# Kernel tuning notes

Measured on AMD Instinct MI355X. Metric: run time of the kernel, lower is better.

The kernel has to match this reference:

```python
import jax, jax.numpy as jnp
import numpy as np

N_WIRES = 4
N_LAYERS = 2
B = 16384
EPS = 1e-5


def apply_ry(state, wire, theta):
    # state: (B,2,2,2,2) complex64; theta: scalar or (B,)
    st = jnp.moveaxis(state, wire + 1, 1)
    half = jnp.asarray(theta) * 0.5
    c = jnp.cos(half).reshape(-1, 1, 1, 1).astype(state.dtype)
    s = jnp.sin(half).reshape(-1, 1, 1, 1).astype(state.dtype)
    n0 = c * st[:, 0] - s * st[:, 1]
    n1 = s * st[:, 0] + c * st[:, 1]
    return jnp.moveaxis(jnp.stack([n0, n1], axis=1), 1, wire + 1)


def apply_rz(state, wire, theta):
    st = jnp.moveaxis(state, wire + 1, 1)
    half = jnp.asarray(theta) * 0.5
    c = jnp.cos(half)
    s = jnp.sin(half)
    p0 = (c - 1j * s).reshape(-1, 1, 1, 1).astype(state.dtype)
    p1 = (c + 1j * s).reshape(-1, 1, 1, 1).astype(state.dtype)
    return jnp.moveaxis(jnp.stack([p0 * st[:, 0], p1 * st[:, 1]], axis=1), 1, wire + 1)


def apply_cnot(state, ctrl, tgt):
    st = jnp.moveaxis(state, (ctrl + 1, tgt + 1), (1, 2))
    # flip target where control == 1
    st = jnp.concatenate([st[:, :1], st[:, 1:, ::-1]], axis=1)
    return jnp.moveaxis(st, (1, 2), (ctrl + 1, tgt + 1))


def expect_z(state):
    probs = jnp.real(state * jnp.conj(state))  # (B,2,2,2,2)
    exps = []
    for w in range(N_WIRES):
        p = jnp.moveaxis(probs, w + 1, 1)
        exps.append((p[:, 0] - p[:, 1]).sum(axis=(1, 2, 3)))
    return jnp.stack(exps, axis=-1)  # (B,4)


def quanv(x, qparams):
    bsz = x.shape[0]
    # 2x2 patches in row-major loop order: (B, 196, 4) with [p00,p01,p10,p11]
    patches = x.reshape(bsz, 14, 2, 14, 2).transpose(0, 1, 3, 2, 4).reshape(bsz, 196, 4)
    patches = jnp.transpose(patches, (1, 0, 2))  # (196, B, 4)
    state0 = jnp.zeros((bsz, 2, 2, 2, 2), jnp.complex64).at[:, 0, 0, 0, 0].set(1.0)

    def step(state, vals):
        # NOTE: original code never resets the device between patches -> state carries over
        for i in range(N_WIRES):
            state = apply_ry(state, i, vals[:, i])
        for l in range(N_LAYERS):
            for i in range(N_WIRES):
                state = apply_ry(state, i, qparams[l, i, 0])
                state = apply_rz(state, i, qparams[l, i, 1])
            for i in range(N_WIRES - 1):
                state = apply_cnot(state, i, i + 1)
        return state, expect_z(state)

    _, meas = jax.lax.scan(step, state0, patches)  # (196, B, 4)
    return jnp.transpose(meas, (1, 0, 2)).reshape(bsz, 196 * 4)


def batchnorm(h, g, b):
    # training-mode BatchNorm1d: biased batch statistics
    m = h.mean(axis=0)
    v = h.var(axis=0)
    return g * (h - m) / jnp.sqrt(v + EPS) + b


def setup_inputs() -> dict:
    key = jax.random.key(0)
    ks = jax.random.split(key, 6)
    x = jax.random.uniform(ks[0], (B, 28, 28), dtype=jnp.float32)
    qparams = jax.random.normal(ks[1], (N_LAYERS, N_WIRES, 2), dtype=jnp.float32)
    w1 = jax.random.normal(ks[2], (256, 784), dtype=jnp.float32) * 0.03
    w2 = jax.random.normal(ks[3], (256, 256), dtype=jnp.float32) * 0.05
    w3 = jax.random.normal(ks[4], (10, 256), dtype=jnp.float32) * 0.05
    return {
        "x": x, "qparams": qparams,
        "w1": w1, "b1": jnp.zeros((256,), jnp.float32),
        "g1": jnp.ones((256,), jnp.float32), "be1": jnp.zeros((256,), jnp.float32),
        "w2": w2, "b2": jnp.zeros((256,), jnp.float32),
        "g2": jnp.ones((256,), jnp.float32), "be2": jnp.zeros((256,), jnp.float32),
        "w3": w3, "b3": jnp.zeros((10,), jnp.float32),
    }


def reference(x, qparams, w1, b1, g1, be1, w2, b2, g2, be2, w3, b3):
    feats = quanv(x, qparams)                      # (B, 784)
    h = jax.nn.relu(batchnorm(feats @ w1.T + b1, g1, be1))
    h2 = jax.nn.relu(batchnorm(h @ w2.T + b2, g2, be2)) + h
    return jax.nn.log_softmax(h2 @ w3.T + b3, axis=-1)
```

## Files before the change

kernel.cpp:

```cpp
#include <hip/hip_runtime.h>
#include <math.h>

#define BQ 16384
#define KFP 800
#define NH 256
#define NCLS 10

typedef float f32x4 __attribute__((ext_vector_type(4)));
typedef unsigned int u32x2 __attribute__((ext_vector_type(2)));
typedef __bf16 bf16x8 __attribute__((ext_vector_type(8)));
typedef __bf16 bf16x4 __attribute__((ext_vector_type(4)));


template<int ST>
__device__ __forceinline__ void u_ry(float* sr, float* si, float c, float s) {
#pragma unroll
  for (int i = 0; i < 16; i++) {
    if (i & ST) continue;
    const int j = i | ST;
    const float a0r = sr[i], a0i = si[i], a1r = sr[j], a1i = si[j];
    sr[i] = c * a0r - s * a1r;  si[i] = c * a0i - s * a1i;
    sr[j] = s * a0r + c * a1r;  si[j] = s * a0i + c * a1i;
  }
}
template<int ST>
__device__ __forceinline__ void u_rz(float* sr, float* si, float c, float s) {
#pragma unroll
  for (int i = 0; i < 16; i++) {
    const float pz = (i & ST) ? s : -s;
    const float ar = sr[i], ai = si[i];
    sr[i] = c * ar - pz * ai;
    si[i] = c * ai + pz * ar;
  }
}
template<int SC, int STG>
__device__ __forceinline__ void u_cnot(float* sr, float* si) {
#pragma unroll
  for (int i = 0; i < 16; i++) {
    if (!(i & SC) || (i & STG)) continue;
    const int j = i | STG;
    float t;
    t = sr[i]; sr[i] = sr[j]; sr[j] = t;
    t = si[i]; si[i] = si[j]; si[j] = t;
  }
}

__global__ __launch_bounds__(256) void prep_kernel(
    const float* __restrict__ qp, const float* __restrict__ w1,
    const float* __restrict__ w2, __bf16* __restrict__ Abuf,
    __bf16* __restrict__ w1b, __bf16* __restrict__ w2b,
    float* __restrict__ gs1, float* __restrict__ gs2) {
  const int bid = blockIdx.x;
  const int tid = threadIdx.x;
  if (bid == 0) {
    gs1[tid] = 0.f; gs1[256 + tid] = 0.f;
    gs2[tid] = 0.f; gs2[256 + tid] = 0.f;
    __shared__ float Ur[16][16], Ui[16][16];
    if (tid < 16) {
      float sr[16], si[16];
#pragma unroll
      for (int i = 0; i < 16; i++) { sr[i] = (i == tid) ? 1.f : 0.f; si[i] = 0.f; }
#pragma unroll
      for (int l = 0; l < 2; l++) {
        { const float t = qp[l*8 + 0] * 0.5f; u_ry<8>(sr, si, cosf(t), sinf(t)); }
        { const float t = qp[l*8 + 1] * 0.5f; u_rz<8>(sr, si, cosf(t), sinf(t)); }
        { const float t = qp[l*8 + 2] * 0.5f; u_ry<4>(sr, si, cosf(t), sinf(t)); }
        { const float t = qp[l*8 + 3] * 0.5f; u_rz<4>(sr, si, cosf(t), sinf(t)); }
        { const float t = qp[l*8 + 4] * 0.5f; u_ry<2>(sr, si, cosf(t), sinf(t)); }
        { const float t = qp[l*8 + 5] * 0.5f; u_rz<2>(sr, si, cosf(t), sinf(t)); }
        { const float t = qp[l*8 + 6] * 0.5f; u_ry<1>(sr, si, cosf(t), sinf(t)); }
        { const float t = qp[l*8 + 7] * 0.5f; u_rz<1>(sr, si, cosf(t), sinf(t)); }
        u_cnot<8, 4>(sr, si);
        u_cnot<4, 2>(sr, si);
        u_cnot<2, 1>(sr, si);
      }
#pragma unroll
      for (int r = 0; r < 16; r++) { Ur[r][tid] = sr[r]; Ui[r][tid] = si[r]; }
    }
    __syncthreads();
    for (int f = tid; f < 2048; f += 256) {
      const int m   = f & 7;
      const int row = (f >> 3) & 15;
      const int kg  = (f >> 7) & 3;
      const int hl  = (f >> 9) & 1;
      const int t   = (f >> 10) & 1;
      const int k   = kg * 8 + m;
      const int ri_o  = (row >> 2) & 1;
      const int amp_o = ((row >> 3) & 1) * 8 + t * 4 + (row & 3);
      const int ri_i  = (k >> 3) & 1;
      const int amp_i = ((k >> 4) & 1) * 8 + (m >> 2) * 4 + (m & 3);
      const float u_r = Ur[amp_o][amp_i], u_i = Ui[amp_o][amp_i];
      float v = (ri_o == 0) ? ((ri_i == 0) ? u_r : -u_i)
                            : ((ri_i == 0) ? u_i : u_r);
      if (hl) {
        const __bf16 hb = (__bf16)v;
        v = v - (float)hb;
      }
      Abuf[f] = (__bf16)v;
    }
  } else if (bid <= 256) {
    const int r = bid - 1;
    for (int c = tid; c < KFP; c += 256)
      w1b[r * KFP + c] = (c < 784) ? (__bf16)w1[r * 784 + c] : (__bf16)0.f;
  } else {
    const int base = (bid - 257) * 2048 + tid * 8;
    const float4 v0 = *(const float4*)(w2 + base);
    const float4 v1 = *(const float4*)(w2 + base + 4);
    bf16x8 o = {(__bf16)v0.x, (__bf16)v0.y, (__bf16)v0.z, (__bf16)v0.w,
                (__bf16)v1.x, (__bf16)v1.y, (__bf16)v1.z, (__bf16)v1.w};
    *(bf16x8*)(w2b + base) = o;
  }
}


__device__ __forceinline__ float swz16(float v) {
  return __int_as_float(__builtin_amdgcn_ds_swizzle(__float_as_int(v), 0x401F));
}
__device__ __forceinline__ float plsum(float v) {
  const u32x2 r = __builtin_amdgcn_permlane32_swap(
      __float_as_uint(v), __float_as_uint(v), false, false);
  return __uint_as_float(r.x) + __uint_as_float(r.y);
}
__device__ __forceinline__ float plpick(float v, bool r0sel) {
  const u32x2 r = __builtin_amdgcn_permlane32_swap(
      __float_as_uint(v), __float_as_uint(v), false, false);
  return __uint_as_float(r0sel ? r.x : r.y);
}

__global__ __launch_bounds__(256) void quanv_mfma(
    const float* __restrict__ x, const __bf16* __restrict__ Abuf,
    __bf16* __restrict__ feats) {
  const int tid = threadIdx.x;
  const int l = tid & 63;
  const int wv = tid >> 6;
  const int col = l & 15;
  const int kg = l >> 4;
  const int b = blockIdx.x * 64 + wv * 16 + col;
  const float* xb = x + (size_t)b * 784;
  __bf16* fb = feats + (size_t)b * KFP;
  const float sg0 = (l & 32) ? 1.f : -1.f;

  const u32x2 pt = __builtin_amdgcn_permlane32_swap((unsigned)l, (unsigned)l,
                                                    false, false);
  const bool p32r0 = (pt.x == (unsigned)(l ^ 32));

  const bf16x8* Ab = (const bf16x8*)Abuf;
  const bf16x8 A0h = Ab[(0 * 4 + kg) * 16 + col];
  const bf16x8 A0l = Ab[(1 * 4 + kg) * 16 + col];
  const bf16x8 A1h = Ab[(2 * 4 + kg) * 16 + col];
  const bf16x8 A1l = Ab[(3 * 4 + kg) * 16 + col];

  f32x4 c0 = {(kg == 0) ? 1.f : 0.f, 0.f, 0.f, 0.f};
  f32x4 c1 = {0.f, 0.f, 0.f, 0.f};
  const f32x4 z4 = {0.f, 0.f, 0.f, 0.f};

  float ts0, tw1, tw2, tw3, gsc;
  auto trig = [&](float2 a, float2 b2) {
    const float h0 = a.x * 0.5f, h1 = a.y * 0.5f;
    const float h2 = b2.x * 0.5f, h3 = b2.y * 0.5f;
    const float c0_ = __cosf(h0), s0_ = __sinf(h0);
    const float c1_ = __cosf(h1), s1_ = __sinf(h1);
    const float c2_ = __cosf(h2), s2_ = __sinf(h2);
    const float c3_ = __cosf(h3), s3_ = __sinf(h3);
    ts0 = sg0 * __fdividef(s0_, c0_);
    tw1 = __fdividef(s1_, c1_);
    tw2 = __fdividef(s2_, c2_);
    tw3 = __fdividef(s3_, c3_);
    gsc = (c0_ * c1_) * (c2_ * c3_);
  };

  auto meas = [&](__bf16* dst) {
    const float sq0 = c0.x * c0.x, sq1 = c0.y * c0.y;
    const float sq2 = c0.z * c0.z, sq3 = c0.w * c0.w;
    const float sq4 = c1.x * c1.x, sq5 = c1.y * c1.y;
    const float sq6 = c1.z * c1.z, sq7 = c1.w * c1.w;
    const float s01 = sq0 + sq1, s23 = sq2 + sq3;
    const float s45 = sq4 + sq5, s67 = sq6 + sq7;
    const float d01 = sq0 - sq1, d23 = sq2 - sq3;
    const float d45 = sq4 - sq5, d67 = sq6 - sq7;
    const float z3 = (d01 + d23) + (d45 + d67);
    const float z2 = (s01 - s23) + (s45 - s67);
    const float q03 = s01 + s23, q47 = s45 + s67;
    const float z1 = q03 - q47;
    const float T  = q03 + q47;
    const float z3a = z3 + swz16(z3);
    const float z2a = z2 + swz16(z2);
    const float z1a = z1 + swz16(z1);
    const float Ta  = -sg0 * (T + swz16(T));
    const float z3f = plsum(z3a);
    const float z2f = plsum(z2a);
    const float z1f = plsum(z1a);
    const float z0f = plsum(Ta);
    if (kg == 0) {
      bf16x4 o = {(__bf16)z0f, (__bf16)z1f, (__bf16)z2f, (__bf16)z3f};
      *(bf16x4*)dst = o;
    }
  };

  auto step = [&]() {
    float S[8] = {c0.x, c0.y, c0.z, c0.w, c1.x, c1.y, c1.z, c1.w};
#pragma unroll
    for (int j = 0; j < 4; j++) {
      const float a = S[j];
      S[j]     = fmaf(-tw1, S[4 + j], S[j]);
      S[4 + j] = fmaf( tw1, a,        S[4 + j]);
    }
#pragma unroll
    for (int base = 0; base < 8; base += 4)
#pragma unroll
      for (int j = 0; j < 2; j++) {
        const int i0 = base + j, i1 = base + j + 2;
        const float a = S[i0];
        S[i0] = fmaf(-tw2, S[i1], S[i0]);
        S[i1] = fmaf( tw2, a,     S[i1]);
      }
#pragma unroll
    for (int i0 = 0; i0 < 8; i0 += 2) {
      const float a = S[i0];
      S[i0]     = fmaf(-tw3, S[i0 + 1], S[i0]);
      S[i0 + 1] = fmaf( tw3, a,         S[i0 + 1]);
    }
#pragma unroll
    for (int i = 0; i < 8; i++) {
      const float P = plpick(S[i], p32r0);
      S[i] = fmaf(ts0, P, S[i]);
    }
    bf16x8 Bh, Bl;
#pragma unroll
    for (int i = 0; i < 8; i++) {
      const float GS = gsc * S[i];
      const __bf16 hb = (__bf16)GS;
      Bh[i] = hb;
      Bl[i] = (__bf16)(GS - (float)hb);
    }
    f32x4 p0 = __builtin_amdgcn_mfma_f32_16x16x32_bf16(A0h, Bh, z4, 0, 0, 0);
    f32x4 q0 = __builtin_amdgcn_mfma_f32_16x16x32_bf16(A0l, Bh, z4, 0, 0, 0);
    q0 = __builtin_amdgcn_mfma_f32_16x16x32_bf16(A0h, Bl, q0, 0, 0, 0);
    f32x4 p1 = __builtin_amdgcn_mfma_f32_16x16x32_bf16(A1h, Bh, z4, 0, 0, 0);
    f32x4 q1 = __builtin_amdgcn_mfma_f32_16x16x32_bf16(A1l, Bh, z4, 0, 0, 0);
    q1 = __builtin_amdgcn_mfma_f32_16x16x32_bf16(A1h, Bl, q1, 0, 0, 0);
    c0 = p0 + q0;
    c1 = p1 + q1;
  };

  float2 t0 = *(const float2*)(xb);
  float2 t1 = *(const float2*)(xb + 28);
  trig(t0, t1);
  t0 = *(const float2*)(xb + 2);
  t1 = *(const float2*)(xb + 30);
  step();
  trig(t0, t1);
  t0 = *(const float2*)(xb + 4);
  t1 = *(const float2*)(xb + 32);
  int nrr = 0, ncc = 3;
  __bf16* fp = fb;

#pragma unroll 2
  for (int it = 1; it < 196; ++it) {
    const float* np = (it < 194) ? (xb + 56 * nrr + 2 * ncc) : xb;
    const float2 n0 = *(const float2*)np;
    const float2 n1 = *(const float2*)(np + 28);
    ncc++;
    if (ncc == 14) { ncc = 0; nrr++; }

    meas(fp); fp += 4;
    step();
    trig(t0, t1);
    t0 = n0; t1 = n1;
  }
  meas(fp);

  if (kg == 0) {
    *(uint4*)(fb + 784) = (uint4){0, 0, 0, 0};
    *(uint4*)(fb + 792) = (uint4){0, 0, 0, 0};
  }
}

#define GBM 128
#define GBN 64
#define GBK 32

__device__ __forceinline__ void gld16(const void* g, void* l) {
  __builtin_amdgcn_global_load_lds(
      (const __attribute__((address_space(1))) unsigned int*)g,
      (__attribute__((address_space(3))) unsigned int*)l, 16, 0, 0);
}

__global__ __launch_bounds__(256) void gemm_bf16_nt(
    const __bf16* __restrict__ A, const __bf16* __restrict__ B,
    const float* __restrict__ bias, float* __restrict__ C,
    int M, int N, int K, float* __restrict__ gstats) {
  __shared__ char lds[24576];
  const int tid = threadIdx.x;
  const int nwg = gridDim.x;
  const int sid = (blockIdx.x & 7) * (nwg >> 3) + (blockIdx.x >> 3);
  const int bm = (sid >> 2) * GBM;
  const int bn = (sid & 3) * GBN;
  const int NK = K / GBK;
  const size_t lda = (size_t)K * 2;

  const int srow = tid >> 2;
  const int lc16 = tid & 3;
  const int ag0 = lc16 ^ ((srow >> 1) & 3);
  const int ag1 = lc16 ^ (((srow + 64) >> 1) & 3);
  const char* a0p = (const char*)A + (size_t)(bm + srow) * lda + ag0 * 16;
  const char* a1p = (const char*)A + (size_t)(bm + 64 + srow) * lda + ag1 * 16;
  const char* b0p = (const char*)B + (size_t)(bn + srow) * lda + ag0 * 16;

  const int wid = tid >> 6, lane = tid & 63;
  const int wr = wid >> 1, wc = wid & 1;
  const int ln15 = lane & 15, ln4 = lane >> 4;
  int aoff[4], boff[2];
#pragma unroll
  for (int m = 0; m < 4; m++) {
    const int row = wr * 64 + m * 16 + ln15;
    aoff[m] = row * 64 + ((ln4 ^ ((row >> 1) & 3)) * 16);
  }
#pragma unroll
  for (int n = 0; n < 2; n++) {
    const int row = wc * 32 + n * 16 + ln15;
    boff[n] = 16384 + row * 64 + ((ln4 ^ ((row >> 1) & 3)) * 16);
  }

  f32x4 acc[4][2];
#pragma unroll
  for (int m = 0; m < 4; m++)
#pragma unroll
    for (int n = 0; n < 2; n++) acc[m][n] = (f32x4){0.f, 0.f, 0.f, 0.f};

  auto stage = [&](int buf, int kt) {
    const size_t kb = (size_t)kt * GBK * 2;
    char* as = lds + buf * 8192 + tid * 16;
    char* bs = lds + 16384 + buf * 4096 + tid * 16;
    gld16(a0p + kb, as);
    gld16(a1p + kb, as + 4096);
    gld16(b0p + kb, bs);
  };

  stage(0, 0);
  for (int kt = 0; kt < NK; kt++) {
    __syncthreads();
    if (kt + 1 < NK) stage((kt + 1) & 1, kt + 1);
    const int ab = (kt & 1) * 8192, bb = (kt & 1) * 4096;
    bf16x8 af[4], bfr[2];
#pragma unroll
    for (int m = 0; m < 4; m++) af[m] = *(const bf16x8*)(lds + ab + aoff[m]);
#pragma unroll
    for (int n = 0; n < 2; n++) bfr[n] = *(const bf16x8*)(lds + bb + boff[n]);
#pragma unroll
    for (int m = 0; m < 4; m++)
#pragma unroll
      for (int n = 0; n < 2; n++)
        acc[m][n] = __builtin_amdgcn_mfma_f32_16x16x32_bf16(af[m], bfr[n], acc[m][n], 0, 0, 0);
  }

  float csum[2], csq[2];
#pragma unroll
  for (int n = 0; n < 2; n++) {
    const int ccol = bn + wc * 32 + n * 16 + ln15;
    const float bv = bias[ccol];
    float s = 0.f, ss = 0.f;
#pragma unroll
    for (int m = 0; m < 4; m++) {
      const int crow = bm + wr * 64 + m * 16 + ln4 * 4;
#pragma unroll
      for (int r = 0; r < 4; r++) {
        const float v = acc[m][n][r] + bv;
        C[(size_t)(crow + r) * N + ccol] = v;
        s += v; ss += v * v;
      }
    }
    csum[n] = s; csq[n] = ss;
  }
  __syncthreads();
  float* sred = (float*)lds;
#pragma unroll
  for (int n = 0; n < 2; n++) {
    const int slot = wid * 128 + ln4 * 32 + n * 16 + ln15;
    sred[slot] = csum[n];
    sred[512 + slot] = csq[n];
  }
  __syncthreads();
  if (tid < 128) {
    const int colb = tid & 63, which = tid >> 6;
    const int wcc = colb >> 5, c31 = colb & 31;
    float a = 0.f;
    const int base = which * 512 + c31;
#pragma unroll
    for (int w2_ = 0; w2_ < 2; w2_++)
#pragma unroll
      for (int l4 = 0; l4 < 4; l4++)
        a += sred[base + (w2_ * 2 + wcc) * 128 + l4 * 32];
    atomicAdd(&gstats[(bn + colb) * 2 + which], a);
  }
}

__global__ __launch_bounds__(256) void bn_finalize_g(
    const float* __restrict__ gstats, const float* __restrict__ g,
    const float* __restrict__ be, float* __restrict__ ab, float* __restrict__ cb) {
  const int t = threadIdx.x;
  const float s = gstats[t * 2], ss = gstats[t * 2 + 1];
  const float mean = s * (1.f / 16384.f);
  const float var = ss * (1.f / 16384.f) - mean * mean;
  const float rstd = rsqrtf(var + 1e-5f);
  const float a = g[t] * rstd;
  ab[t] = a;
  cb[t] = be[t] - mean * a;
}

__global__ __launch_bounds__(256) void bn_relu_cvt(
    const float* __restrict__ h, __bf16* __restrict__ hb,
    const float* __restrict__ ab, const float* __restrict__ cb) {
  const size_t i = (size_t)blockIdx.x * 256 + threadIdx.x;
  const float4 v = ((const float4*)h)[i];
  const int col = (int)((i * 4) & (NH - 1));
  const float4 a = *(const float4*)(ab + col);
  const float4 c = *(const float4*)(cb + col);
  bf16x4 o = {(__bf16)fmaxf(fmaf(v.x, a.x, c.x), 0.f),
              (__bf16)fmaxf(fmaf(v.y, a.y, c.y), 0.f),
              (__bf16)fmaxf(fmaf(v.z, a.z, c.z), 0.f),
              (__bf16)fmaxf(fmaf(v.w, a.w, c.w), 0.f)};
  *(bf16x4*)(hb + i * 4) = o;
}

__global__ __launch_bounds__(256) void tail_fused(
    const float* __restrict__ h2p, const __bf16* __restrict__ h1b,
    const float* __restrict__ ab, const float* __restrict__ cb,
    const float* __restrict__ w3, const float* __restrict__ b3,
    float* __restrict__ out) {
  __shared__ float w3s[NCLS * NH];
  __shared__ float as[NH], cs[NH];
  for (int i = threadIdx.x; i < NCLS * NH; i += 256) w3s[i] = w3[i];
  as[threadIdx.x] = ab[threadIdx.x];
  cs[threadIdx.x] = cb[threadIdx.x];
  __syncthreads();

  const int m = blockIdx.x * 256 + threadIdx.x;
  const float* hr = h2p + (size_t)m * NH;
  const __bf16* rr = h1b + (size_t)m * NH;
  float acc[NCLS];
#pragma unroll
  for (int n = 0; n < NCLS; n++) acc[n] = b3[n];

  for (int k = 0; k < NH; k += 8) {
    const float4 hv0 = *(const float4*)(hr + k);
    const float4 hv1 = *(const float4*)(hr + k + 4);
    const bf16x8 rv = *(const bf16x8*)(rr + k);
    float v[8] = {hv0.x, hv0.y, hv0.z, hv0.w, hv1.x, hv1.y, hv1.z, hv1.w};
#pragma unroll
    for (int j = 0; j < 8; j++)
      v[j] = fmaxf(fmaf(v[j], as[k + j], cs[k + j]), 0.f) + (float)rv[j];
#pragma unroll
    for (int n = 0; n < NCLS; n++) {
      float d = 0.f;
#pragma unroll
      for (int j = 0; j < 8; j++) d = fmaf(v[j], w3s[n * NH + k + j], d);
      acc[n] += d;
    }
  }

  float mx = acc[0];
#pragma unroll
  for (int n = 1; n < NCLS; n++) mx = fmaxf(mx, acc[n]);
  float se = 0.f;
#pragma unroll
  for (int n = 0; n < NCLS; n++) se += expf(acc[n] - mx);
  const float lse = logf(se) + mx;
#pragma unroll
  for (int n = 0; n < NCLS; n++) out[(size_t)m * NCLS + n] = acc[n] - lse;
}

extern "C" void kernel_launch(void* const* d_in, const int* in_sizes, int n_in,
                              void* d_out, int out_size, void* d_ws, size_t ws_size,
                              hipStream_t stream) {
  const float* x   = (const float*)d_in[0];
  const float* qp  = (const float*)d_in[1];
  const float* w1  = (const float*)d_in[2];
  const float* b1  = (const float*)d_in[3];
  const float* g1  = (const float*)d_in[4];
  const float* be1 = (const float*)d_in[5];
  const float* w2  = (const float*)d_in[6];
  const float* b2  = (const float*)d_in[7];
  const float* g2  = (const float*)d_in[8];
  const float* be2 = (const float*)d_in[9];
  const float* w3  = (const float*)d_in[10];
  const float* b3  = (const float*)d_in[11];
  float* out = (float*)d_out;

  char* w = (char*)d_ws;
  __bf16* feats = (__bf16*)w;
  float*  h1    = (float*)(w + 26214400);
  float*  h2p   = (float*)(w + 42991616);
  __bf16* h1b   = (__bf16*)(w + 59768832);
  __bf16* w1b   = (__bf16*)(w + 68157440);
  __bf16* w2b   = (__bf16*)(w + 68567040);
  float*  gs1   = (float*)(w + 68698112);
  float*  gs2   = (float*)(w + 68700160);
  float*  ab1   = (float*)(w + 68702208);
  float*  cb1   = (float*)(w + 68703232);
  float*  ab2   = (float*)(w + 68704256);
  float*  cb2   = (float*)(w + 68705280);
  __bf16* Abuf  = (__bf16*)(w + 68706304);

  prep_kernel<<<289, 256, 0, stream>>>(qp, w1, w2, Abuf, w1b, w2b, gs1, gs2);
  quanv_mfma<<<BQ / 64, 256, 0, stream>>>(x, Abuf, feats);

  gemm_bf16_nt<<<(BQ / GBM) * (NH / GBN), 256, 0, stream>>>(
      feats, w1b, b1, h1, BQ, NH, KFP, gs1);
  bn_finalize_g<<<1, 256, 0, stream>>>(gs1, g1, be1, ab1, cb1);
  bn_relu_cvt<<<(BQ * NH / 4) / 256, 256, 0, stream>>>(h1, h1b, ab1, cb1);

  gemm_bf16_nt<<<(BQ / GBM) * (NH / GBN), 256, 0, stream>>>(
      h1b, w2b, b2, h2p, BQ, NH, NH, gs2);
  bn_finalize_g<<<1, 256, 0, stream>>>(gs2, g2, be2, ab2, cb2);

  tail_fused<<<BQ / 256, 256, 0, stream>>>(h2p, h1b, ab2, cb2, w3, b3, out);
}
```

Measured before the change: 202.4 us.

## Interleave two independent quanv sample groups per wavefront to hide serial latency

The quanv kernel now has each 64-lane wavefront process two groups of 16 samples at once, interleaving their measure/step/trig chains. Previously each wave carried one serial dependency chain of MFMA, permlane and trig work across 196 patches. Interleaving two independent chains is meant to let one group's MFMA and cross-lane latency overlap with the other's ALU work. Launch geometry changes from 256-thread blocks of 64 samples to 64-thread blocks of 32 samples, so the total wave count halves and register pressure per wave rises, which can reduce occupancy.

```diff
diff --git a/kernel.cpp b/kernel.cpp
--- a/kernel.cpp
+++ b/kernel.cpp
@@ -127,17 +127,116 @@
   return __uint_as_float(r0sel ? r.x : r.y);
 }
 
-__global__ __launch_bounds__(256) void quanv_mfma(
+struct QGrp {
+  f32x4 c0, c1;
+  float ts0, tw1, tw2, tw3, gsc;
+  float2 t0, t1;
+  const float* xb;
+  __bf16* fb;
+};
+
+__device__ __forceinline__ void q_trig(QGrp& g, float2 a, float2 b2, float sg0) {
+  const float h0 = a.x * 0.5f, h1 = a.y * 0.5f;
+  const float h2 = b2.x * 0.5f, h3 = b2.y * 0.5f;
+  const float c0_ = __cosf(h0), s0_ = __sinf(h0);
+  const float c1_ = __cosf(h1), s1_ = __sinf(h1);
+  const float c2_ = __cosf(h2), s2_ = __sinf(h2);
+  const float c3_ = __cosf(h3), s3_ = __sinf(h3);
+  g.ts0 = sg0 * __fdividef(s0_, c0_);
+  g.tw1 = __fdividef(s1_, c1_);
+  g.tw2 = __fdividef(s2_, c2_);
+  g.tw3 = __fdividef(s3_, c3_);
+  g.gsc = (c0_ * c1_) * (c2_ * c3_);
+}
+
+__device__ __forceinline__ void q_meas(const QGrp& g, __bf16* dst,
+                                       float sg0, int kg) {
+  const f32x4 c0 = g.c0, c1 = g.c1;
+  const float sq0 = c0.x * c0.x, sq1 = c0.y * c0.y;
+  const float sq2 = c0.z * c0.z, sq3 = c0.w * c0.w;
+  const float sq4 = c1.x * c1.x, sq5 = c1.y * c1.y;
+  const float sq6 = c1.z * c1.z, sq7 = c1.w * c1.w;
+  const float s01 = sq0 + sq1, s23 = sq2 + sq3;
+  const float s45 = sq4 + sq5, s67 = sq6 + sq7;
+  const float d01 = sq0 - sq1, d23 = sq2 - sq3;
+  const float d45 = sq4 - sq5, d67 = sq6 - sq7;
+  const float z3 = (d01 + d23) + (d45 + d67);
+  const float z2 = (s01 - s23) + (s45 - s67);
+  const float q03 = s01 + s23, q47 = s45 + s67;
+  const float z1 = q03 - q47;
+  const float T  = q03 + q47;
+  const float z3a = z3 + swz16(z3);
+  const float z2a = z2 + swz16(z2);
+  const float z1a = z1 + swz16(z1);
+  const float Ta  = -sg0 * (T + swz16(T));
+  const float z3f = plsum(z3a);
+  const float z2f = plsum(z2a);
+  const float z1f = plsum(z1a);
+  const float z0f = plsum(Ta);
+  if (kg == 0) {
+    bf16x4 o = {(__bf16)z0f, (__bf16)z1f, (__bf16)z2f, (__bf16)z3f};
+    *(bf16x4*)dst = o;
+  }
+}
+
+__device__ __forceinline__ void q_step(QGrp& g, bool p32r0,
+                                       bf16x8 A0h, bf16x8 A0l,
+                                       bf16x8 A1h, bf16x8 A1l) {
+  const f32x4 z4 = {0.f, 0.f, 0.f, 0.f};
+  float S[8] = {g.c0.x, g.c0.y, g.c0.z, g.c0.w,
+                g.c1.x, g.c1.y, g.c1.z, g.c1.w};
+#pragma unroll
+  for (int j = 0; j < 4; j++) {
+    const float a = S[j];
+    S[j]     = fmaf(-g.tw1, S[4 + j], S[j]);
+    S[4 + j] = fmaf( g.tw1, a,        S[4 + j]);
+  }
+#pragma unroll
+  for (int base = 0; base < 8; base += 4)
+#pragma unroll
+    for (int j = 0; j < 2; j++) {
+      const int i0 = base + j, i1 = base + j + 2;
+      const float a = S[i0];
+      S[i0] = fmaf(-g.tw2, S[i1], S[i0]);
+      S[i1] = fmaf( g.tw2, a,     S[i1]);
+    }
+#pragma unroll
+  for (int i0 = 0; i0 < 8; i0 += 2) {
+    const float a = S[i0];
+    S[i0]     = fmaf(-g.tw3, S[i0 + 1], S[i0]);
+    S[i0 + 1] = fmaf( g.tw3, a,         S[i0 + 1]);
+  }
+#pragma unroll
+  for (int i = 0; i < 8; i++) {
+    const float P = plpick(S[i], p32r0);
+    S[i] = fmaf(g.ts0, P, S[i]);
+  }
+  bf16x8 Bh, Bl;
+#pragma unroll
+  for (int i = 0; i < 8; i++) {
+    const float GS = g.gsc * S[i];
+    const __bf16 hb = (__bf16)GS;
+    Bh[i] = hb;
+    Bl[i] = (__bf16)(GS - (float)hb);
+  }
+  f32x4 p0 = __builtin_amdgcn_mfma_f32_16x16x32_bf16(A0h, Bh, z4, 0, 0, 0);
+  f32x4 q0 = __builtin_amdgcn_mfma_f32_16x16x32_bf16(A0l, Bh, z4, 0, 0, 0);
+  q0 = __builtin_amdgcn_mfma_f32_16x16x32_bf16(A0h, Bl, q0, 0, 0, 0);
+  f32x4 p1 = __builtin_amdgcn_mfma_f32_16x16x32_bf16(A1h, Bh, z4, 0, 0, 0);
+  f32x4 q1 = __builtin_amdgcn_mfma_f32_16x16x32_bf16(A1l, Bh, z4, 0, 0, 0);
+  q1 = __builtin_amdgcn_mfma_f32_16x16x32_bf16(A1h, Bl, q1, 0, 0, 0);
+  g.c0 = p0 + q0;
+  g.c1 = p1 + q1;
+}
+
+__global__ __launch_bounds__(64) void quanv_mfma(
     const float* __restrict__ x, const __bf16* __restrict__ Abuf,
     __bf16* __restrict__ feats) {
-  const int tid = threadIdx.x;
-  const int l = tid & 63;
-  const int wv = tid >> 6;
+  const int l = threadIdx.x;
   const int col = l & 15;
   const int kg = l >> 4;
-  const int b = blockIdx.x * 64 + wv * 16 + col;
-  const float* xb = x + (size_t)b * 784;
-  __bf16* fb = feats + (size_t)b * KFP;
+  const int bA = blockIdx.x * 32 + col;
+  const int bB = bA + 16;
   const float sg0 = (l & 32) ? 1.f : -1.f;
 
   const u32x2 pt = __builtin_amdgcn_permlane32_swap((unsigned)l, (unsigned)l,
@@ -150,129 +249,59 @@
   const bf16x8 A1h = Ab[(2 * 4 + kg) * 16 + col];
   const bf16x8 A1l = Ab[(3 * 4 + kg) * 16 + col];
 
-  f32x4 c0 = {(kg == 0) ? 1.f : 0.f, 0.f, 0.f, 0.f};
-  f32x4 c1 = {0.f, 0.f, 0.f, 0.f};
-  const f32x4 z4 = {0.f, 0.f, 0.f, 0.f};
-
-  float ts0, tw1, tw2, tw3, gsc;
-  auto trig = [&](float2 a, float2 b2) {
-    const float h0 = a.x * 0.5f, h1 = a.y * 0.5f;
-    const float h2 = b2.x * 0.5f, h3 = b2.y * 0.5f;
-    const float c0_ = __cosf(h0), s0_ = __sinf(h0);
-    const float c1_ = __cosf(h1), s1_ = __sinf(h1);
-    const float c2_ = __cosf(h2), s2_ = __sinf(h2);
-    const float c3_ = __cosf(h3), s3_ = __sinf(h3);
-    ts0 = sg0 * __fdividef(s0_, c0_);
-    tw1 = __fdividef(s1_, c1_);
-    tw2 = __fdividef(s2_, c2_);
-    tw3 = __fdividef(s3_, c3_);
-    gsc = (c0_ * c1_) * (c2_ * c3_);
-  };
-
-  auto meas = [&](__bf16* dst) {
-    const float sq0 = c0.x * c0.x, sq1 = c0.y * c0.y;
-    const float sq2 = c0.z * c0.z, sq3 = c0.w * c0.w;
-    const float sq4 = c1.x * c1.x, sq5 = c1.y * c1.y;
-    const float sq6 = c1.z * c1.z, sq7 = c1.w * c1.w;
-    const float s01 = sq0 + sq1, s23 = sq2 + sq3;
-    const float s45 = sq4 + sq5, s67 = sq6 + sq7;
-    const float d01 = sq0 - sq1, d23 = sq2 - sq3;
-    const float d45 = sq4 - sq5, d67 = sq6 - sq7;
-    const float z3 = (d01 + d23) + (d45 + d67);
-    const float z2 = (s01 - s23) + (s45 - s67);
-    const float q03 = s01 + s23, q47 = s45 + s67;
-    const float z1 = q03 - q47;
-    const float T  = q03 + q47;
-    const float z3a = z3 + swz16(z3);
-    const float z2a = z2 + swz16(z2);
-    const float z1a = z1 + swz16(z1);
-    const float Ta  = -sg0 * (T + swz16(T));
-    const float z3f = plsum(z3a);
-    const float z2f = plsum(z2a);
-    const float z1f = plsum(z1a);
-    const float z0f = plsum(Ta);
-    if (kg == 0) {
-      bf16x4 o = {(__bf16)z0f, (__bf16)z1f, (__bf16)z2f, (__bf16)z3f};
-      *(bf16x4*)dst = o;
-    }
-  };
-
-  auto step = [&]() {
-    float S[8] = {c0.x, c0.y, c0.z, c0.w, c1.x, c1.y, c1.z, c1.w};
-#pragma unroll
-    for (int j = 0; j < 4; j++) {
-      const float a = S[j];
-      S[j]     = fmaf(-tw1, S[4 + j], S[j]);
-      S[4 + j] = fmaf( tw1, a,        S[4 + j]);
-    }
-#pragma unroll
-    for (int base = 0; base < 8; base += 4)
-#pragma unroll
-      for (int j = 0; j < 2; j++) {
-        const int i0 = base + j, i1 = base + j + 2;
-        const float a = S[i0];
-        S[i0] = fmaf(-tw2, S[i1], S[i0]);
-        S[i1] = fmaf( tw2, a,     S[i1]);
-      }
-#pragma unroll
-    for (int i0 = 0; i0 < 8; i0 += 2) {
-      const float a = S[i0];
-      S[i0]     = fmaf(-tw3, S[i0 + 1], S[i0]);
-      S[i0 + 1] = fmaf( tw3, a,         S[i0 + 1]);
-    }
-#pragma unroll
-    for (int i = 0; i < 8; i++) {
-      const float P = plpick(S[i], p32r0);
-      S[i] = fmaf(ts0, P, S[i]);
-    }
-    bf16x8 Bh, Bl;
-#pragma unroll
-    for (int i = 0; i < 8; i++) {
-      const float GS = gsc * S[i];
-      const __bf16 hb = (__bf16)GS;
-      Bh[i] = hb;
-      Bl[i] = (__bf16)(GS - (float)hb);
-    }
-    f32x4 p0 = __builtin_amdgcn_mfma_f32_16x16x32_bf16(A0h, Bh, z4, 0, 0, 0);
-    f32x4 q0 = __builtin_amdgcn_mfma_f32_16x16x32_bf16(A0l, Bh, z4, 0, 0, 0);
-    q0 = __builtin_amdgcn_mfma_f32_16x16x32_bf16(A0h, Bl, q0, 0, 0, 0);
-    f32x4 p1 = __builtin_amdgcn_mfma_f32_16x16x32_bf16(A1h, Bh, z4, 0, 0, 0);
-    f32x4 q1 = __builtin_amdgcn_mfma_f32_16x16x32_bf16(A1l, Bh, z4, 0, 0, 0);
-    q1 = __builtin_amdgcn_mfma_f32_16x16x32_bf16(A1h, Bl, q1, 0, 0, 0);
-    c0 = p0 + q0;
-    c1 = p1 + q1;
-  };
-
-  float2 t0 = *(const float2*)(xb);
-  float2 t1 = *(const float2*)(xb + 28);
-  trig(t0, t1);
-  t0 = *(const float2*)(xb + 2);
-  t1 = *(const float2*)(xb + 30);
-  step();
-  trig(t0, t1);
-  t0 = *(const float2*)(xb + 4);
-  t1 = *(const float2*)(xb + 32);
+  QGrp A, B;
+  A.xb = x + (size_t)bA * 784;  A.fb = feats + (size_t)bA * KFP;
+  B.xb = x + (size_t)bB * 784;  B.fb = feats + (size_t)bB * KFP;
+  A.c0 = (f32x4){(kg == 0) ? 1.f : 0.f, 0.f, 0.f, 0.f};
+  A.c1 = (f32x4){0.f, 0.f, 0.f, 0.f};
+  B.c0 = A.c0; B.c1 = A.c1;
+
+  {
+    const float2 a0 = *(const float2*)(A.xb);
+    const float2 a1 = *(const float2*)(A.xb + 28);
+    const float2 b0 = *(const float2*)(B.xb);
+    const float2 b1 = *(const float2*)(B.xb + 28);
+    q_trig(A, a0, a1, sg0);
+    q_trig(B, b0, b1, sg0);
+  }
+  A.t0 = *(const float2*)(A.xb + 2);  A.t1 = *(const float2*)(A.xb + 30);
+  B.t0 = *(const float2*)(B.xb + 2);  B.t1 = *(const float2*)(B.xb + 30);
+  q_step(A, p32r0, A0h, A0l, A1h, A1l);
+  q_step(B, p32r0, A0h, A0l, A1h, A1l);
+  q_trig(A, A.t0, A.t1, sg0);
+  q_trig(B, B.t0, B.t1, sg0);
+  A.t0 = *(const float2*)(A.xb + 4);  A.t1 = *(const float2*)(A.xb + 32);
+  B.t0 = *(const float2*)(B.xb + 4);  B.t1 = *(const float2*)(B.xb + 32);
   int nrr = 0, ncc = 3;
-  __bf16* fp = fb;
-
-#pragma unroll 2
+  __bf16* fpA = A.fb;
+  __bf16* fpB = B.fb;
+
   for (int it = 1; it < 196; ++it) {
-    const float* np = (it < 194) ? (xb + 56 * nrr + 2 * ncc) : xb;
-    const float2 n0 = *(const float2*)np;
-    const float2 n1 = *(const float2*)(np + 28);
+    const int off = (it < 194) ? (56 * nrr + 2 * ncc) : 0;
+    const float2 nA0 = *(const float2*)(A.xb + off);
+    const float2 nA1 = *(const float2*)(A.xb + off + 28);
+    const float2 nB0 = *(const float2*)(B.xb + off);
+    const float2 nB1 = *(const float2*)(B.xb + off + 28);
     ncc++;
     if (ncc == 14) { ncc = 0; nrr++; }
 
-    meas(fp); fp += 4;
-    step();
-    trig(t0, t1);
-    t0 = n0; t1 = n1;
-  }
-  meas(fp);
+    q_meas(A, fpA, sg0, kg); fpA += 4;
+    q_meas(B, fpB, sg0, kg); fpB += 4;
+    q_step(A, p32r0, A0h, A0l, A1h, A1l);
+    q_step(B, p32r0, A0h, A0l, A1h, A1l);
+    q_trig(A, A.t0, A.t1, sg0);
+    q_trig(B, B.t0, B.t1, sg0);
+    A.t0 = nA0; A.t1 = nA1;
+    B.t0 = nB0; B.t1 = nB1;
+  }
+  q_meas(A, fpA, sg0, kg);
+  q_meas(B, fpB, sg0, kg);
 
   if (kg == 0) {
-    *(uint4*)(fb + 784) = (uint4){0, 0, 0, 0};
-    *(uint4*)(fb + 792) = (uint4){0, 0, 0, 0};
+    *(uint4*)(A.fb + 784) = (uint4){0, 0, 0, 0};
+    *(uint4*)(A.fb + 792) = (uint4){0, 0, 0, 0};
+    *(uint4*)(B.fb + 784) = (uint4){0, 0, 0, 0};
+    *(uint4*)(B.fb + 792) = (uint4){0, 0, 0, 0};
   }
 }
 
@@ -503,7 +532,7 @@
   __bf16* Abuf  = (__bf16*)(w + 68706304);
 
   prep_kernel<<<289, 256, 0, stream>>>(qp, w1, w2, Abuf, w1b, w2b, gs1, gs2);
-  quanv_mfma<<<BQ / 64, 256, 0, stream>>>(x, Abuf, feats);
+  quanv_mfma<<<BQ / 32, 64, 0, stream>>>(x, Abuf, feats);
 
   gemm_bf16_nt<<<(BQ / GBM) * (NH / GBN), 256, 0, stream>>>(
       feats, w1b, b1, h1, BQ, NH, KFP, gs1);
```

Result: slower. 293.8 us (+45.1%).

## Store GEMM outputs as bf16 and fold BN finalize into consumers

Applied to the files above, without the earlier changes.

The GEMM epilogue now writes pre-activation outputs as bf16 instead of fp32, which halves the write traffic and the read traffic of the following BN/ReLU and tail kernels. The separate one-block bn_finalize launches are removed, and each consumer block recomputes mean and rstd from the global stats into shared memory, saving two launches. The quanv kernel's hi/lo bf16 split now uses bit masking and v_perm packing instead of float-to-bf16 converts. In exchange, pre-BN values lose precision, and the hi part is now truncated rather than rounded (the lo residual compensates).

```diff
diff --git a/kernel.cpp b/kernel.cpp
--- a/kernel.cpp
+++ b/kernel.cpp
@@ -8,6 +8,7 @@
 
 typedef float f32x4 __attribute__((ext_vector_type(4)));
 typedef unsigned int u32x2 __attribute__((ext_vector_type(2)));
+typedef unsigned int u32x4 __attribute__((ext_vector_type(4)));
 typedef __bf16 bf16x8 __attribute__((ext_vector_type(8)));
 typedef __bf16 bf16x4 __attribute__((ext_vector_type(4)));
 
@@ -225,14 +226,22 @@
       const float P = plpick(S[i], p32r0);
       S[i] = fmaf(ts0, P, S[i]);
     }
-    bf16x8 Bh, Bl;
+    unsigned gb[8], lb[8];
 #pragma unroll
     for (int i = 0; i < 8; i++) {
       const float GS = gsc * S[i];
-      const __bf16 hb = (__bf16)GS;
-      Bh[i] = hb;
-      Bl[i] = (__bf16)(GS - (float)hb);
-    }
+      const unsigned bb = __float_as_uint(GS);
+      gb[i] = bb;
+      lb[i] = __float_as_uint(GS - __uint_as_float(bb & 0xFFFF0000u));
+    }
+    u32x4 bhv, blv;
+#pragma unroll
+    for (int j = 0; j < 4; j++) {
+      bhv[j] = __builtin_amdgcn_perm(gb[2 * j + 1], gb[2 * j], 0x07060302u);
+      blv[j] = __builtin_amdgcn_perm(lb[2 * j + 1], lb[2 * j], 0x07060302u);
+    }
+    const bf16x8 Bh = __builtin_bit_cast(bf16x8, bhv);
+    const bf16x8 Bl = __builtin_bit_cast(bf16x8, blv);
     f32x4 p0 = __builtin_amdgcn_mfma_f32_16x16x32_bf16(A0h, Bh, z4, 0, 0, 0);
     f32x4 q0 = __builtin_amdgcn_mfma_f32_16x16x32_bf16(A0l, Bh, z4, 0, 0, 0);
     q0 = __builtin_amdgcn_mfma_f32_16x16x32_bf16(A0h, Bl, q0, 0, 0, 0);
@@ -288,7 +297,7 @@
 
 __global__ __launch_bounds__(256) void gemm_bf16_nt(
     const __bf16* __restrict__ A, const __bf16* __restrict__ B,
-    const float* __restrict__ bias, float* __restrict__ C,
+    const float* __restrict__ bias, __bf16* __restrict__ C,
     int M, int N, int K, float* __restrict__ gstats) {
   __shared__ char lds[24576];
   const int tid = threadIdx.x;
@@ -366,7 +375,7 @@
 #pragma unroll
       for (int r = 0; r < 4; r++) {
         const float v = acc[m][n][r] + bv;
-        C[(size_t)(crow + r) * N + ccol] = v;
+        C[(size_t)(crow + r) * N + ccol] = (__bf16)v;
         s += v; ss += v * v;
       }
     }
@@ -395,61 +404,64 @@
   }
 }
 
-__global__ __launch_bounds__(256) void bn_finalize_g(
+__global__ __launch_bounds__(256) void bn1_relu(
+    const __bf16* __restrict__ h1p, __bf16* __restrict__ h1b,
     const float* __restrict__ gstats, const float* __restrict__ g,
-    const float* __restrict__ be, float* __restrict__ ab, float* __restrict__ cb) {
-  const int t = threadIdx.x;
-  const float s = gstats[t * 2], ss = gstats[t * 2 + 1];
-  const float mean = s * (1.f / 16384.f);
-  const float var = ss * (1.f / 16384.f) - mean * mean;
-  const float rstd = rsqrtf(var + 1e-5f);
-  const float a = g[t] * rstd;
-  ab[t] = a;
-  cb[t] = be[t] - mean * a;
-}
-
-__global__ __launch_bounds__(256) void bn_relu_cvt(
-    const float* __restrict__ h, __bf16* __restrict__ hb,
-    const float* __restrict__ ab, const float* __restrict__ cb) {
+    const float* __restrict__ be) {
+  __shared__ float as[NH], cs[NH];
+  {
+    const int t = threadIdx.x;
+    const float s = gstats[t * 2], ss = gstats[t * 2 + 1];
+    const float mean = s * (1.f / 16384.f);
+    const float var = ss * (1.f / 16384.f) - mean * mean;
+    const float a = g[t] * rsqrtf(var + 1e-5f);
+    as[t] = a;
+    cs[t] = be[t] - mean * a;
+  }
+  __syncthreads();
   const size_t i = (size_t)blockIdx.x * 256 + threadIdx.x;
-  const float4 v = ((const float4*)h)[i];
-  const int col = (int)((i * 4) & (NH - 1));
-  const float4 a = *(const float4*)(ab + col);
-  const float4 c = *(const float4*)(cb + col);
-  bf16x4 o = {(__bf16)fmaxf(fmaf(v.x, a.x, c.x), 0.f),
-              (__bf16)fmaxf(fmaf(v.y, a.y, c.y), 0.f),
-              (__bf16)fmaxf(fmaf(v.z, a.z, c.z), 0.f),
-              (__bf16)fmaxf(fmaf(v.w, a.w, c.w), 0.f)};
-  *(bf16x4*)(hb + i * 4) = o;
+  const bf16x8 v = *(const bf16x8*)(h1p + i * 8);
+  const int colb = (int)((i * 8) & (NH - 1));
+  bf16x8 o;
+#pragma unroll
+  for (int j = 0; j < 8; j++)
+    o[j] = (__bf16)fmaxf(fmaf((float)v[j], as[colb + j], cs[colb + j]), 0.f);
+  *(bf16x8*)(h1b + i * 8) = o;
 }
 
 __global__ __launch_bounds__(256) void tail_fused(
-    const float* __restrict__ h2p, const __bf16* __restrict__ h1b,
-    const float* __restrict__ ab, const float* __restrict__ cb,
-    const float* __restrict__ w3, const float* __restrict__ b3,
-    float* __restrict__ out) {
+    const __bf16* __restrict__ h2b, const __bf16* __restrict__ h1b,
+    const float* __restrict__ gstats, const float* __restrict__ g,
+    const float* __restrict__ be, const float* __restrict__ w3,
+    const float* __restrict__ b3, float* __restrict__ out) {
   __shared__ float w3s[NCLS * NH];
   __shared__ float as[NH], cs[NH];
   for (int i = threadIdx.x; i < NCLS * NH; i += 256) w3s[i] = w3[i];
-  as[threadIdx.x] = ab[threadIdx.x];
-  cs[threadIdx.x] = cb[threadIdx.x];
+  {
+    const int t = threadIdx.x;
+    const float s = gstats[t * 2], ss = gstats[t * 2 + 1];
+    const float mean = s * (1.f / 16384.f);
+    const float var = ss * (1.f / 16384.f) - mean * mean;
+    const float a = g[t] * rsqrtf(var + 1e-5f);
+    as[t] = a;
+    cs[t] = be[t] - mean * a;
+  }
   __syncthreads();
 
   const int m = blockIdx.x * 256 + threadIdx.x;
-  const float* hr = h2p + (size_t)m * NH;
+  const __bf16* hr = h2b + (size_t)m * NH;
   const __bf16* rr = h1b + (size_t)m * NH;
   float acc[NCLS];
 #pragma unroll
   for (int n = 0; n < NCLS; n++) acc[n] = b3[n];
 
   for (int k = 0; k < NH; k += 8) {
-    const float4 hv0 = *(const float4*)(hr + k);
-    const float4 hv1 = *(const float4*)(hr + k + 4);
+    const bf16x8 hv = *(const bf16x8*)(hr + k);
     const bf16x8 rv = *(const bf16x8*)(rr + k);
-    float v[8] = {hv0.x, hv0.y, hv0.z, hv0.w, hv1.x, hv1.y, hv1.z, hv1.w};
+    float v[8];
 #pragma unroll
     for (int j = 0; j < 8; j++)
-      v[j] = fmaxf(fmaf(v[j], as[k + j], cs[k + j]), 0.f) + (float)rv[j];
+      v[j] = fmaxf(fmaf((float)hv[j], as[k + j], cs[k + j]), 0.f) + (float)rv[j];
 #pragma unroll
     for (int n = 0; n < NCLS; n++) {
       float d = 0.f;
@@ -489,30 +501,24 @@
 
   char* w = (char*)d_ws;
   __bf16* feats = (__bf16*)w;
-  float*  h1    = (float*)(w + 26214400);
-  float*  h2p   = (float*)(w + 42991616);
-  __bf16* h1b   = (__bf16*)(w + 59768832);
-  __bf16* w1b   = (__bf16*)(w + 68157440);
-  __bf16* w2b   = (__bf16*)(w + 68567040);
-  float*  gs1   = (float*)(w + 68698112);
-  float*  gs2   = (float*)(w + 68700160);
-  float*  ab1   = (float*)(w + 68702208);
-  float*  cb1   = (float*)(w + 68703232);
-  float*  ab2   = (float*)(w + 68704256);
-  float*  cb2   = (float*)(w + 68705280);
-  __bf16* Abuf  = (__bf16*)(w + 68706304);
+  __bf16* h1p   = (__bf16*)(w + 26214400);
+  __bf16* h1b   = (__bf16*)(w + 34603008);
+  __bf16* h2b   = (__bf16*)(w + 42991616);
+  __bf16* w1b   = (__bf16*)(w + 51380224);
+  __bf16* w2b   = (__bf16*)(w + 51789824);
+  float*  gs1   = (float*)(w + 51920896);
+  float*  gs2   = (float*)(w + 51922944);
+  __bf16* Abuf  = (__bf16*)(w + 51924992);
 
   prep_kernel<<<289, 256, 0, stream>>>(qp, w1, w2, Abuf, w1b, w2b, gs1, gs2);
   quanv_mfma<<<BQ / 64, 256, 0, stream>>>(x, Abuf, feats);
 
   gemm_bf16_nt<<<(BQ / GBM) * (NH / GBN), 256, 0, stream>>>(
-      feats, w1b, b1, h1, BQ, NH, KFP, gs1);
-  bn_finalize_g<<<1, 256, 0, stream>>>(gs1, g1, be1, ab1, cb1);
-  bn_relu_cvt<<<(BQ * NH / 4) / 256, 256, 0, stream>>>(h1, h1b, ab1, cb1);
+      feats, w1b, b1, h1p, BQ, NH, KFP, gs1);
+  bn1_relu<<<(BQ * NH / 8) / 256, 256, 0, stream>>>(h1p, h1b, gs1, g1, be1);
 
   gemm_bf16_nt<<<(BQ / GBM) * (NH / GBN), 256, 0, stream>>>(
-      h1b, w2b, b2, h2p, BQ, NH, NH, gs2);
-  bn_finalize_g<<<1, 256, 0, stream>>>(gs2, g2, be2, ab2, cb2);
-
-  tail_fused<<<BQ / 256, 256, 0, stream>>>(h2p, h1b, ab2, cb2, w3, b3, out);
-}
+      h1b, w2b, b2, h2b, BQ, NH, NH, gs2);
+
+  tail_fused<<<BQ / 256, 256, 0, stream>>>(h2b, h1b, gs2, g2, be2, w3, b3, out);
+}
```

Measured after the change: 205.9 us. Within noise of the previous version (+1.7%).
